# Optimization experiments

Measured on AMD Instinct MI355X. Metric: run time of the kernel, lower is better.

Reference implementation:

```python
import jax, jax.numpy as jnp
import numpy as np

EPS = 1e-15


def setup_inputs() -> dict:
    key = jax.random.key(0)
    k1, k2, k3 = jax.random.split(key, 3)
    B, F, C, T = 8, 257, 8, 3000
    X_real = jax.random.normal(k1, (B, F, C, T), dtype=jnp.float32)
    X_imag = jax.random.normal(k2, (B, F, C, T), dtype=jnp.float32)
    mask = jax.random.uniform(k3, (B, F, T), dtype=jnp.float32)
    return {"X_real": X_real, "X_imag": X_imag, "mask": mask}


def reference(X_real, X_imag, mask):
    # X: (B, F, C, T) complex STFT
    X = X_real + 1j * X_imag
    # normalize mask over time (normalize=True)
    m = mask / (jnp.sum(mask, axis=-1, keepdims=True) + EPS)  # (B,F,T)
    # Fused masked time-weighted outer product: equivalent to
    # einsum('...ct,...et->...tce') * mask then sum over t, but contracts
    # t directly (batched GEMM) without the (B,F,T,C,C) intermediate.
    Xm = X * m[..., None, :]                                  # (B,F,C,T)
    psd = jnp.einsum('bfct,bfet->bfce', Xm, jnp.conj(X))      # (B,F,C,C)
    return psd
```

## Files before the change

kernel.cpp:

```cpp
#include <hip/hip_runtime.h>

#define T_LEN 3000
#define C_CH 8
#define NTHREADS 256
#define NWAVES 4
#define TT 256
#define NCHUNK 12
#define NSTREAM 17

#define AS1 __attribute__((address_space(1)))
#define AS3 __attribute__((address_space(3)))
#define GLOAD_LDS(G, L) \
    __builtin_amdgcn_global_load_lds((const AS1 void*)(G), (AS3 void*)(L), 16, 0, 0)

#define XPOSE_ROUND(OFF)                                        \
    {                                                           \
        const bool hi = (lane & (OFF)) != 0;                    \
        _Pragma("unroll")                                       \
        for (int i = 0; i < (OFF); ++i) {                       \
            float send = hi ? acc[i] : acc[i + (OFF)];          \
            float recv = __shfl_xor(send, (OFF));               \
            float keep = hi ? acc[i + (OFF)] : acc[i];          \
            acc[i] = keep + recv;                               \
        }                                                       \
    }

__device__ __forceinline__ void stage(const float* __restrict__ Xr,
                                      const float* __restrict__ Xi,
                                      const float* __restrict__ Mk,
                                      float* buf, int slice, int off,
                                      int wave, int lane) {
    int elem = off + lane * 4;
    if (elem > T_LEN - 4) elem = T_LEN - 4;
    const size_t xbase = (size_t)slice * (C_CH * T_LEN);
#pragma unroll
    for (int k = 0; k < 4; ++k) {
        const int s = wave + 4 * k;
        const float* g = (s < 8)
            ? (Xr + xbase + (size_t)s * T_LEN + elem)
            : (Xi + xbase + (size_t)(s - 8) * T_LEN + elem);
        GLOAD_LDS(g, buf + s * TT);
    }
    if (wave == 0) {
        const float* g = Mk + (size_t)slice * T_LEN + elem;
        GLOAD_LDS(g, buf + 16 * TT);
    }
}

__global__ __launch_bounds__(NTHREADS, 4) void psd_kernel(
        const float* __restrict__ Xr,
        const float* __restrict__ Xi,
        const float* __restrict__ Mk,
        float* __restrict__ out,
        int real_elems, int write_imag) {
    const int slice = blockIdx.x;
    const int tid   = threadIdx.x;
    const int lane  = tid & 63;
    const int wave  = tid >> 6;

    __shared__ float lds[2][NSTREAM * TT];
    __shared__ float red[NWAVES * 64];
    __shared__ float sred[NWAVES];
    __shared__ float fin[128];

    float acc[64];
#pragma unroll
    for (int k = 0; k < 64; ++k) acc[k] = 0.f;
    float s = 0.f;

    stage(Xr, Xi, Mk, lds[0], slice, 0, wave, lane);

    for (int ch = 0; ch < NCHUNK; ++ch) {
        const int cur = ch & 1;
        if (ch + 1 < NCHUNK) {
            stage(Xr, Xi, Mk, lds[cur ^ 1], slice, (ch + 1) * TT, wave, lane);
            if (wave == 0) asm volatile("s_waitcnt vmcnt(5)" ::: "memory");
            else           asm volatile("s_waitcnt vmcnt(4)" ::: "memory");
        } else {
            asm volatile("s_waitcnt vmcnt(0)" ::: "memory");
        }
        __builtin_amdgcn_s_barrier();

        const int rem   = T_LEN - ch * TT;
        const int valid = rem < TT ? rem : TT;
        const float* buf = lds[cur];
        if (tid < valid) {
            const float m = buf[16 * TT + tid];
            s += m;
            float xr[C_CH], xi[C_CH];
#pragma unroll
            for (int c = 0; c < C_CH; ++c) {
                xr[c] = buf[c * TT + tid];
                xi[c] = buf[(8 + c) * TT + tid];
            }
            float mr[C_CH], mi[C_CH];
#pragma unroll
            for (int c = 0; c < C_CH; ++c) {
                mr[c] = m * xr[c];
                mi[c] = m * xi[c];
            }
#pragma unroll
            for (int c = 0; c < C_CH; ++c)
                acc[c] += mr[c] * xr[c] + mi[c] * xi[c];
#pragma unroll
            for (int c = 0; c < C_CH; ++c) {
#pragma unroll
                for (int e = c + 1; e < C_CH; ++e) {
                    const int p = 7 * c - (c * (c - 1)) / 2 + (e - c - 1);
                    acc[8 + p]  += mr[c] * xr[e] + mi[c] * xi[e];
                    acc[36 + p] += mi[c] * xr[e] - mr[c] * xi[e];
                }
            }
        }
        asm volatile("" ::: "memory");
        __builtin_amdgcn_s_barrier();
    }

#pragma unroll
    for (int off = 32; off > 0; off >>= 1) s += __shfl_xor(s, off);

    XPOSE_ROUND(32)
    XPOSE_ROUND(16)
    XPOSE_ROUND(8)
    XPOSE_ROUND(4)
    XPOSE_ROUND(2)
    XPOSE_ROUND(1)

    red[wave * 64 + lane] = acc[0];
    if (lane == 0) sred[wave] = s;
    __syncthreads();

    if (tid < 64) {
        float tot = (red[tid] + red[64 + tid]) + (red[128 + tid] + red[192 + tid]);
        const float stot = (sred[0] + sred[1]) + (sred[2] + sred[3]);
        tot *= 1.0f / (stot + 1e-15f);

        if (tid < 8) {
            const int c = tid;
            fin[c * 8 + c]      = tot;
            fin[64 + c * 8 + c] = 0.f;
        } else {
            int p = (tid < 36) ? (tid - 8) : (tid - 36);
            int c = 0;
            while (p >= 7 - c) { p -= 7 - c; ++c; }
            const int e = c + 1 + p;
            if (tid < 36) {
                fin[c * 8 + e] = tot;
                fin[e * 8 + c] = tot;
            } else {
                fin[64 + c * 8 + e] = tot;
                fin[64 + e * 8 + c] = -tot;
            }
        }
    }
    __syncthreads();
    if (tid < 64) {
        out[(size_t)slice * 64 + tid] = fin[tid];
    } else if (tid < 128 && write_imag) {
        out[(size_t)real_elems + (size_t)slice * 64 + (tid - 64)] = fin[tid];
    }
}

extern "C" void kernel_launch(void* const* d_in, const int* in_sizes, int n_in,
                              void* d_out, int out_size, void* d_ws, size_t ws_size,
                              hipStream_t stream) {
    const float* Xr = (const float*)d_in[0];
    const float* Xi = (const float*)d_in[1];
    const float* Mk = (const float*)d_in[2];
    float* out = (float*)d_out;
    const int slices = in_sizes[2] / T_LEN;
    const int real_elems = slices * 64;
    const int write_imag = (out_size >= 2 * real_elems) ? 1 : 0;
    psd_kernel<<<dim3(slices), dim3(NTHREADS), 0, stream>>>(Xr, Xi, Mk, out,
                                                            real_elems, write_imag);
}
```

Baseline: 410.6 us.

## Split time axis across blocks with workspace partials and a combine kernel

After: 436.3 us. +6.3%, slower.

```diff
diff --git a/kernel.cpp b/kernel.cpp
--- a/kernel.cpp
+++ b/kernel.cpp
@@ -5,7 +5,6 @@
 #define NTHREADS 256
 #define NWAVES 4
 #define TT 256
-#define NCHUNK 12
 #define NSTREAM 17
 
 #define AS1 __attribute__((address_space(1)))
@@ -47,13 +46,20 @@
     }
 }
 
-__global__ __launch_bounds__(NTHREADS, 4) void psd_kernel(
+__global__ __launch_bounds__(NTHREADS, 4) void psd_partial(
         const float* __restrict__ Xr,
         const float* __restrict__ Xi,
         const float* __restrict__ Mk,
+        float* __restrict__ ws,
         float* __restrict__ out,
+        int tsplit, int tpb, int direct,
         int real_elems, int write_imag) {
-    const int slice = blockIdx.x;
+    const int blk   = blockIdx.x;
+    const int slice = blk / tsplit;
+    const int tb    = blk - slice * tsplit;
+    const int t0    = tb * tpb;
+    const int trem  = (T_LEN - t0 < tpb) ? (T_LEN - t0) : tpb;
+    const int nch   = (trem + TT - 1) / TT;
     const int tid   = threadIdx.x;
     const int lane  = tid & 63;
     const int wave  = tid >> 6;
@@ -68,12 +74,12 @@
     for (int k = 0; k < 64; ++k) acc[k] = 0.f;
     float s = 0.f;
 
-    stage(Xr, Xi, Mk, lds[0], slice, 0, wave, lane);
-
-    for (int ch = 0; ch < NCHUNK; ++ch) {
+    stage(Xr, Xi, Mk, lds[0], slice, t0, wave, lane);
+
+    for (int ch = 0; ch < nch; ++ch) {
         const int cur = ch & 1;
-        if (ch + 1 < NCHUNK) {
-            stage(Xr, Xi, Mk, lds[cur ^ 1], slice, (ch + 1) * TT, wave, lane);
+        if (ch + 1 < nch) {
+            stage(Xr, Xi, Mk, lds[cur ^ 1], slice, t0 + (ch + 1) * TT, wave, lane);
             if (wave == 0) asm volatile("s_waitcnt vmcnt(5)" ::: "memory");
             else           asm volatile("s_waitcnt vmcnt(4)" ::: "memory");
         } else {
@@ -81,7 +87,7 @@
         }
         __builtin_amdgcn_s_barrier();
 
-        const int rem   = T_LEN - ch * TT;
+        const int rem   = trem - ch * TT;
         const int valid = rem < TT ? rem : TT;
         const float* buf = lds[cur];
         if (tid < valid) {
@@ -130,11 +136,20 @@
     if (lane == 0) sred[wave] = s;
     __syncthreads();
 
+    if (!direct) {
+        if (tid < 64) {
+            float tot = (red[tid] + red[64 + tid]) + (red[128 + tid] + red[192 + tid]);
+            ws[(size_t)blk * 65 + tid] = tot;
+        } else if (tid == 64) {
+            ws[(size_t)blk * 65 + 64] = (sred[0] + sred[1]) + (sred[2] + sred[3]);
+        }
+        return;
+    }
+
     if (tid < 64) {
         float tot = (red[tid] + red[64 + tid]) + (red[128 + tid] + red[192 + tid]);
         const float stot = (sred[0] + sred[1]) + (sred[2] + sred[3]);
         tot *= 1.0f / (stot + 1e-15f);
-
         if (tid < 8) {
             const int c = tid;
             fin[c * 8 + c]      = tot;
@@ -144,13 +159,8 @@
             int c = 0;
             while (p >= 7 - c) { p -= 7 - c; ++c; }
             const int e = c + 1 + p;
-            if (tid < 36) {
-                fin[c * 8 + e] = tot;
-                fin[e * 8 + c] = tot;
-            } else {
-                fin[64 + c * 8 + e] = tot;
-                fin[64 + e * 8 + c] = -tot;
-            }
+            if (tid < 36) { fin[c * 8 + e] = tot;      fin[e * 8 + c] = tot; }
+            else          { fin[64 + c * 8 + e] = tot; fin[64 + e * 8 + c] = -tot; }
         }
     }
     __syncthreads();
@@ -159,6 +169,40 @@
     } else if (tid < 128 && write_imag) {
         out[(size_t)real_elems + (size_t)slice * 64 + (tid - 64)] = fin[tid];
     }
+}
+
+__global__ __launch_bounds__(64) void psd_combine(
+        const float* __restrict__ ws,
+        float* __restrict__ out,
+        int tsplit, int real_elems, int write_imag) {
+    const int slice = blockIdx.x;
+    const int tid   = threadIdx.x;
+    __shared__ float fin[128];
+
+    float tot = 0.f, stot = 0.f;
+    for (int j = 0; j < tsplit; ++j) {
+        const size_t base = (size_t)(slice * tsplit + j) * 65;
+        tot  += ws[base + tid];
+        stot += ws[base + 64];
+    }
+    tot *= 1.0f / (stot + 1e-15f);
+
+    if (tid < 8) {
+        const int c = tid;
+        fin[c * 8 + c]      = tot;
+        fin[64 + c * 8 + c] = 0.f;
+    } else {
+        int p = (tid < 36) ? (tid - 8) : (tid - 36);
+        int c = 0;
+        while (p >= 7 - c) { p -= 7 - c; ++c; }
+        const int e = c + 1 + p;
+        if (tid < 36) { fin[c * 8 + e] = tot;      fin[e * 8 + c] = tot; }
+        else          { fin[64 + c * 8 + e] = tot; fin[64 + e * 8 + c] = -tot; }
+    }
+    __syncthreads();
+    out[(size_t)slice * 64 + tid] = fin[tid];
+    if (write_imag)
+        out[(size_t)real_elems + (size_t)slice * 64 + tid] = fin[64 + tid];
 }
 
 extern "C" void kernel_launch(void* const* d_in, const int* in_sizes, int n_in,
@@ -168,9 +212,21 @@
     const float* Xi = (const float*)d_in[1];
     const float* Mk = (const float*)d_in[2];
     float* out = (float*)d_out;
+    float* ws  = (float*)d_ws;
     const int slices = in_sizes[2] / T_LEN;
     const int real_elems = slices * 64;
     const int write_imag = (out_size >= 2 * real_elems) ? 1 : 0;
-    psd_kernel<<<dim3(slices), dim3(NTHREADS), 0, stream>>>(Xr, Xi, Mk, out,
-                                                            real_elems, write_imag);
-}
+
+    int tsplit = 4;
+    while (tsplit > 1 && ws_size < (size_t)slices * tsplit * 65 * sizeof(float))
+        tsplit >>= 1;
+    const int direct = (ws_size < (size_t)slices * 65 * sizeof(float)) ? 1 : 0;
+    if (direct) tsplit = 1;
+    const int tpb = (T_LEN + tsplit - 1) / tsplit;
+
+    psd_partial<<<dim3(slices * tsplit), dim3(NTHREADS), 0, stream>>>(
+        Xr, Xi, Mk, ws, out, tsplit, tpb, direct, real_elems, write_imag);
+    if (!direct)
+        psd_combine<<<dim3(slices), dim3(64), 0, stream>>>(
+            ws, out, tsplit, real_elems, write_imag);
+}
```
